# Performance work log

Measured on AMD Instinct MI355X. Metric: run time of the kernel, lower is better.

## Reference

```python
import jax, jax.numpy as jnp
import numpy as np

N_NODES = 50000
N_EDGES = 800000
OUT_DIM = 394
BN_EPS = 1e-5


def setup_inputs() -> dict:
    key = jax.random.key(0)
    ks = jax.random.split(key, 10)
    x = jax.random.normal(ks[0], (N_NODES, 2), dtype=jnp.float32)
    edge_index = jax.random.randint(ks[1], (2, N_EDGES), 0, N_NODES, dtype=jnp.int64)
    W_gcn = jax.random.normal(ks[2], (OUT_DIM, 2), dtype=jnp.float32) * 0.5
    b_gcn = jax.random.normal(ks[3], (OUT_DIM,), dtype=jnp.float32) * 0.1
    bn_gamma = jax.random.normal(ks[4], (OUT_DIM,), dtype=jnp.float32) * 0.1 + 1.0
    bn_beta = jax.random.normal(ks[5], (OUT_DIM,), dtype=jnp.float32) * 0.1
    bn_mean = jax.random.normal(ks[6], (OUT_DIM,), dtype=jnp.float32) * 0.1
    bn_var = jax.random.uniform(ks[7], (OUT_DIM,), dtype=jnp.float32, minval=0.5, maxval=1.5)
    fc_w = jax.random.normal(ks[8], (OUT_DIM, OUT_DIM), dtype=jnp.float32) * (1.0 / np.sqrt(OUT_DIM))
    fc_b = jax.random.normal(ks[9], (OUT_DIM,), dtype=jnp.float32) * 0.1
    return {"x": x, "edge_index": edge_index, "W_gcn": W_gcn, "b_gcn": b_gcn,
            "bn_gamma": bn_gamma, "bn_beta": bn_beta, "bn_mean": bn_mean,
            "bn_var": bn_var, "fc_w": fc_w, "fc_b": fc_b}


def reference(x, edge_index, W_gcn, b_gcn, bn_gamma, bn_beta, bn_mean, bn_var, fc_w, fc_b):
    n = x.shape[0]
    loop = jnp.arange(n, dtype=edge_index.dtype)
    # PyG GCNConv: add self-loops, symmetric deg^{-1/2} normalization
    src = jnp.concatenate([edge_index[0], loop])  # [E+N] message sources
    dst = jnp.concatenate([edge_index[1], loop])  # [E+N] message targets
    deg = jax.ops.segment_sum(jnp.ones_like(dst, dtype=x.dtype), dst, num_segments=n)
    dinv = jnp.where(deg > 0, jax.lax.rsqrt(deg), 0.0)
    norm = dinv[src] * dinv[dst]  # [E+N]
    xl = x @ W_gcn.T  # [N, 394] linear transform before aggregation
    msgs = xl[src] * norm[:, None]  # [E+N, 394] gathered + normalized messages
    agg = jax.ops.segment_sum(msgs, dst, num_segments=n) + b_gcn  # scatter-add
    h = jax.nn.relu(agg)
    # BatchNorm1d in eval mode (running stats)
    h = (h - bn_mean) * jax.lax.rsqrt(bn_var + BN_EPS) * bn_gamma + bn_beta
    # dropout is a no-op in eval mode
    z = h @ fc_w.T + fc_b
    return (jax.nn.log_softmax(z, axis=1), z)
```

## Files before the change

kernel.cpp:

```cpp
#include <hip/hip_runtime.h>
#include <math.h>

#define DIM 394
#define KP  416
#define NT  13
#define NP  448
#define BN_EPS 1e-5f
#define MAXD 32

typedef __bf16 bf16x8 __attribute__((ext_vector_type(8)));
typedef float  f32x4  __attribute__((ext_vector_type(4)));

__device__ inline bool edges_are_int32(const int* ei) {
    int l = threadIdx.x & 63;
    unsigned long long b = __ballot(ei[2 * l + 1] != 0);
    return b != 0ULL;
}


__global__ void place_pack_kernel(const int* __restrict__ ei,
                                  unsigned* __restrict__ degc,
                                  unsigned* __restrict__ payload,
                                  unsigned* __restrict__ ocnt,
                                  uint2* __restrict__ olist, int e, int eb4,
                                  const float* __restrict__ Wg,
                                  const float* __restrict__ bg,
                                  const float* __restrict__ gamma,
                                  const float* __restrict__ beta,
                                  const float* __restrict__ mean,
                                  const float* __restrict__ var,
                                  const float* __restrict__ fcw,
                                  float4* __restrict__ Pk, float* __restrict__ Ok,
                                  bf16x8* __restrict__ Bp) {
    int b = blockIdx.x, t = threadIdx.x;
    if (b < eb4) {
        bool is32 = edges_are_int32(ei);
        int i0 = (b * 256 + t) * 4;
        if (i0 >= e) return;
        int s[4], d[4];
        int cnt = 4;
        if (i0 + 4 <= e) {
            if (is32) {
                int4 sv = *reinterpret_cast<const int4*>(&ei[i0]);
                int4 dv = *reinterpret_cast<const int4*>(&ei[e + i0]);
                s[0] = sv.x; s[1] = sv.y; s[2] = sv.z; s[3] = sv.w;
                d[0] = dv.x; d[1] = dv.y; d[2] = dv.z; d[3] = dv.w;
            } else {
                int4 a = *reinterpret_cast<const int4*>(&ei[2 * i0]);
                int4 bb = *reinterpret_cast<const int4*>(&ei[2 * i0 + 4]);
                int4 c = *reinterpret_cast<const int4*>(&ei[2 * (e + i0)]);
                int4 dd = *reinterpret_cast<const int4*>(&ei[2 * (e + i0) + 4]);
                s[0] = a.x; s[1] = a.z; s[2] = bb.x; s[3] = bb.z;
                d[0] = c.x; d[1] = c.z; d[2] = dd.x; d[3] = dd.z;
            }
        } else {
            cnt = e - i0;
            for (int j = 0; j < cnt; ++j) {
                s[j] = is32 ? ei[i0 + j]     : ei[2 * (i0 + j)];
                d[j] = is32 ? ei[e + i0 + j] : ei[2 * (e + i0 + j)];
            }
        }
        #pragma unroll
        for (int j = 0; j < 4; ++j) {
            if (j >= cnt) break;
            unsigned tk = atomicAdd(&degc[d[j]], 1u);
            if (tk < MAXD) {
                payload[(size_t)d[j] * MAXD + tk] = (unsigned)s[j];
            } else {
                unsigned o = atomicAdd(ocnt, 1u);
                olist[o] = make_uint2((unsigned)s[j], (unsigned)d[j]);
            }
        }
    } else if (b < eb4 + 2) {
        int k = (b - eb4) * 256 + t;
        if (k < KP) {
            float4 p = make_float4(0.f, 0.f, 0.f, 0.f);
            float o = 0.f;
            if (k < DIM) {
                p.x = Wg[2 * k];
                p.y = Wg[2 * k + 1];
                p.z = bg[k];
                float sc = gamma[k] * rsqrtf(var[k] + BN_EPS);
                p.w = sc;
                o = beta[k] - sc * mean[k];
            }
            Pk[k] = p;
            Ok[k] = o;
        }
    } else {
        int idx = (b - eb4 - 2) * 256 + t;
        if (idx < NT * 4 * NP) {
            int col = idx % NP;
            int r   = idx / NP;
            int k0  = r * 8;
            bf16x8 v;
            #pragma unroll
            for (int q = 0; q < 8; ++q) {
                int k = k0 + q;
                float f = (col < DIM && k < DIM) ? fcw[col * DIM + k] : 0.0f;
                v[q] = (__bf16)f;
            }
            Bp[idx] = v;
        }
    }
}

__global__ __launch_bounds__(256, 2)
void gemm_fused(const float2* __restrict__ x2, const unsigned* __restrict__ degc,
                const unsigned* __restrict__ payload,
                const unsigned* __restrict__ ocnt, const uint2* __restrict__ olist,
                const float4* __restrict__ Pk, const float* __restrict__ Ok,
                const bf16x8* __restrict__ Bp, const float* __restrict__ fcb,
                float* __restrict__ outp, float* __restrict__ z, int n) {
    __shared__ bf16x8 As[2][256];
    __shared__ float2 red[64][4];

    int tid = threadIdx.x;
    int wv  = tid >> 6;
    int l   = tid & 63;
    int cg_ = tid & 15;
    int kg  = l >> 4;
    int row0 = blockIdx.x * 64;
    int gi = row0 + l;

    float y0 = 0.f, y1 = 0.f;
    {
        float2 psum = make_float2(0.f, 0.f);
        float dinv_i = 0.f;
        float2 xi = make_float2(0.f, 0.f);
        if (gi < n) {
            unsigned dg = degc[gi];
            dinv_i = rsqrtf(1.0f + (float)dg);
            xi = x2[gi];
            unsigned m = dg < MAXD ? dg : MAXD;
            const unsigned* pl = payload + (size_t)gi * MAXD;
            for (unsigned t = wv; t < m; t += 4) {
                unsigned s = pl[t];
                float2 xv = x2[s];
                float ds = rsqrtf(1.0f + (float)degc[s]);
                psum.x = fmaf(ds, xv.x, psum.x);
                psum.y = fmaf(ds, xv.y, psum.y);
            }
            if (wv == 0) {
                unsigned cnt = *ocnt;
                for (unsigned j = 0; j < cnt; ++j) {
                    uint2 sd = olist[j];
                    if ((int)sd.y == gi) {
                        float2 xv = x2[sd.x];
                        float ds = rsqrtf(1.0f + (float)degc[sd.x]);
                        psum.x = fmaf(ds, xv.x, psum.x);
                        psum.y = fmaf(ds, xv.y, psum.y);
                    }
                }
            }
        }
        red[l][wv] = psum;
        __syncthreads();
        if (gi < n) {
            float sx = red[l][0].x + red[l][1].x + red[l][2].x + red[l][3].x;
            float sy = red[l][0].y + red[l][1].y + red[l][2].y + red[l][3].y;
            y0 = dinv_i * (sx + dinv_i * xi.x);
            y1 = dinv_i * (sy + dinv_i * xi.y);
        }
    }

    f32x4 acc[4][7];
    #pragma unroll
    for (int a = 0; a < 4; ++a)
        #pragma unroll
        for (int b = 0; b < 7; ++b)
            acc[a][b] = (f32x4){0.f, 0.f, 0.f, 0.f};

    auto stageA = [&](int ks, int buf) {
        int kb = ks * 32 + wv * 8;
        bf16x8 hv;
        #pragma unroll
        for (int q = 0; q < 8; ++q) {
            float4 p = Pk[kb + q];
            float t = fmaf(y0, p.x, fmaf(y1, p.y, p.z));
            t = fmaxf(t, 0.f);
            hv[q] = (__bf16)fmaf(p.w, t, Ok[kb + q]);
        }
        As[buf][wv * 64 + l] = hv;
    };

    const bf16x8* bptr = Bp + (kg * 448 + wv * 112 + cg_);

    bf16x8 Bcur[7], Bnxt[7];
    #pragma unroll
    for (int c = 0; c < 7; ++c) Bcur[c] = bptr[c * 16];
    stageA(0, 0);
    __syncthreads();

    int buf = 0;
    for (int ks = 0; ks < NT; ++ks) {
        if (ks < NT - 1) {
            const bf16x8* bn = bptr + (size_t)(ks + 1) * (4 * 448);
            #pragma unroll
            for (int c = 0; c < 7; ++c) Bnxt[c] = bn[c * 16];
            stageA(ks + 1, buf ^ 1);
        }
        bf16x8 af[4];
        #pragma unroll
        for (int rt = 0; rt < 4; ++rt)
            af[rt] = As[buf][kg * 64 + rt * 16 + cg_];
        #pragma unroll
        for (int ct = 0; ct < 7; ++ct)
            #pragma unroll
            for (int rt = 0; rt < 4; ++rt)
                acc[rt][ct] = __builtin_amdgcn_mfma_f32_16x16x32_bf16(
                                  af[rt], Bcur[ct], acc[rt][ct], 0, 0, 0);
        __syncthreads();
        #pragma unroll
        for (int c = 0; c < 7; ++c) Bcur[c] = Bnxt[c];
        buf ^= 1;
    }

    float* redm = (float*)&As[0][0];
    float* reds = redm + 256;

    int colb = wv * 112;
    float bias[7];
    bool  cv[7];
    #pragma unroll
    for (int ct = 0; ct < 7; ++ct) {
        int c = colb + ct * 16 + cg_;
        cv[ct] = (c < DIM);
        bias[ct] = cv[ct] ? fcb[c] : 0.f;
    }
    #pragma unroll
    for (int rt = 0; rt < 4; ++rt)
        #pragma unroll
        for (int ct = 0; ct < 7; ++ct)
            acc[rt][ct] = acc[rt][ct] + bias[ct];

    f32x4 mx[4];
    #pragma unroll
    for (int rt = 0; rt < 4; ++rt) {
        f32x4 m = (f32x4){-1e30f, -1e30f, -1e30f, -1e30f};
        #pragma unroll
        for (int ct = 0; ct < 7; ++ct) {
            if (!cv[ct]) continue;
            #pragma unroll
            for (int j = 0; j < 4; ++j) m[j] = fmaxf(m[j], acc[rt][ct][j]);
        }
        #pragma unroll
        for (int msk = 1; msk < 16; msk <<= 1)
            #pragma unroll
            for (int j = 0; j < 4; ++j)
                m[j] = fmaxf(m[j], __shfl_xor(m[j], msk));
        mx[rt] = m;
    }
    if (cg_ == 0) {
        #pragma unroll
        for (int rt = 0; rt < 4; ++rt)
            #pragma unroll
            for (int j = 0; j < 4; ++j)
                redm[(rt * 16 + kg * 4 + j) * 4 + wv] = mx[rt][j];
    }
    __syncthreads();
    f32x4 gm[4];
    #pragma unroll
    for (int rt = 0; rt < 4; ++rt)
        #pragma unroll
        for (int j = 0; j < 4; ++j) {
            int r = (rt * 16 + kg * 4 + j) * 4;
            gm[rt][j] = fmaxf(fmaxf(redm[r], redm[r + 1]),
                              fmaxf(redm[r + 2], redm[r + 3]));
        }

    f32x4 sm[4];
    #pragma unroll
    for (int rt = 0; rt < 4; ++rt) {
        f32x4 s = (f32x4){0.f, 0.f, 0.f, 0.f};
        #pragma unroll
        for (int ct = 0; ct < 7; ++ct) {
            if (!cv[ct]) continue;
            #pragma unroll
            for (int j = 0; j < 4; ++j)
                s[j] += __expf(acc[rt][ct][j] - gm[rt][j]);
        }
        #pragma unroll
        for (int msk = 1; msk < 16; msk <<= 1)
            #pragma unroll
            for (int j = 0; j < 4; ++j)
                s[j] += __shfl_xor(s[j], msk);
        sm[rt] = s;
    }
    if (cg_ == 0) {
        #pragma unroll
        for (int rt = 0; rt < 4; ++rt)
            #pragma unroll
            for (int j = 0; j < 4; ++j)
                reds[(rt * 16 + kg * 4 + j) * 4 + wv] = sm[rt][j];
    }
    __syncthreads();
    f32x4 lse[4];
    #pragma unroll
    for (int rt = 0; rt < 4; ++rt)
        #pragma unroll
        for (int j = 0; j < 4; ++j) {
            int r = (rt * 16 + kg * 4 + j) * 4;
            float t = reds[r] + reds[r + 1] + reds[r + 2] + reds[r + 3];
            lse[rt][j] = gm[rt][j] + __logf(t);
        }

    #pragma unroll
    for (int rt = 0; rt < 4; ++rt)
        #pragma unroll
        for (int j = 0; j < 4; ++j) {
            int grow = row0 + rt * 16 + kg * 4 + j;
            if (grow >= n) continue;
            size_t base = (size_t)grow * DIM;
            float L = lse[rt][j];
            #pragma unroll
            for (int ct = 0; ct < 7; ++ct) {
                if (!cv[ct]) continue;
                int c = colb + ct * 16 + cg_;
                float zv = acc[rt][ct][j];
                z[base + c]    = zv;
                outp[base + c] = zv - L;
            }
        }
}

extern "C" void kernel_launch(void* const* d_in, const int* in_sizes, int n_in,
                              void* d_out, int out_size, void* d_ws, size_t ws_size,
                              hipStream_t stream) {
    int n = in_sizes[0] / 2;
    int e = in_sizes[1] / 2;

    const float2* x2   = (const float2*)d_in[0];
    const int*   ei    = (const int*)d_in[1];
    const float* Wg    = (const float*)d_in[2];
    const float* bg    = (const float*)d_in[3];
    const float* gamma = (const float*)d_in[4];
    const float* beta  = (const float*)d_in[5];
    const float* mean  = (const float*)d_in[6];
    const float* var   = (const float*)d_in[7];
    const float* fcw   = (const float*)d_in[8];
    const float* fcb   = (const float*)d_in[9];

    float* out = (float*)d_out;
    float* z   = out + (size_t)n * DIM;

    char* wsb = (char*)d_ws;
    unsigned* degc  = (unsigned*)wsb;
    unsigned* ocnt  = (unsigned*)(degc + n);
    uint2*    olist = (uint2*)(ocnt + 4);
    size_t off = (size_t)(n + 4) * 4 + (size_t)e * 8;
    off = (off + 255) & ~(size_t)255;
    unsigned* payload = (unsigned*)(wsb + off);
    off += (size_t)n * MAXD * 4;
    off = (off + 255) & ~(size_t)255;
    bf16x8* Bp = (bf16x8*)(wsb + off);
    off += (size_t)NT * 4 * NP * 16;
    float4* Pk = (float4*)(wsb + off);
    off += (size_t)KP * 16;
    float* Ok  = (float*)(wsb + off);

    hipMemsetAsync(degc, 0, (size_t)(n + 4) * 4, stream);

    int eb4 = (e / 4 + 255) / 256 + 1;
    int pack_blocks = 2 + (NT * 4 * NP + 255) / 256;
    place_pack_kernel<<<eb4 + pack_blocks, 256, 0, stream>>>(
        ei, degc, payload, ocnt, olist, e, eb4,
        Wg, bg, gamma, beta, mean, var, fcw, Pk, Ok, Bp);

    int gm = (n + 63) / 64;
    gemm_fused<<<gm, 256, 0, stream>>>(x2, degc, payload, ocnt, olist,
                                       Pk, Ok, Bp, fcb, out, z, n);
}
```

Before: 139.9 us.

## Scatter overflow edges in separate kernel and stage output through LDS for coalesced stores

Overflow edges (degree beyond MAXD) are no longer scanned linearly by every row in the GEMM kernel. A new cleanup kernel atomically adds their contributions into a per-node yover buffer, which the GEMM reads directly. The epilogue also transposes each 16-row tile through shared memory so z and log-softmax outputs are written as contiguous float2 row segments instead of strided scalar stores. This adds a kernel launch, a larger memset and extra barriers, and the larger shared footprint may reduce occupancy.

```diff
diff --git a/kernel.cpp b/kernel.cpp
--- a/kernel.cpp
+++ b/kernel.cpp
@@ -7,6 +7,7 @@
 #define NP  448
 #define BN_EPS 1e-5f
 #define MAXD 32
+#define TST 452
 
 typedef __bf16 bf16x8 __attribute__((ext_vector_type(8)));
 typedef float  f32x4  __attribute__((ext_vector_type(4)));
@@ -105,15 +106,33 @@
     }
 }
 
+__global__ void cleanup_kernel(const uint2* __restrict__ olist,
+                               const unsigned* __restrict__ ocnt,
+                               const unsigned* __restrict__ degc,
+                               const float2* __restrict__ x2,
+                               float* __restrict__ yover) {
+    unsigned cnt = *ocnt;
+    int gstride = gridDim.x * blockDim.x;
+    for (unsigned i = blockIdx.x * blockDim.x + threadIdx.x; i < cnt; i += gstride) {
+        uint2 sd = olist[i];
+        float ds = rsqrtf(1.0f + (float)degc[sd.x]);
+        float2 xv = x2[sd.x];
+        atomicAdd(&yover[2 * sd.y],     ds * xv.x);
+        atomicAdd(&yover[2 * sd.y + 1], ds * xv.y);
+    }
+}
+
 __global__ __launch_bounds__(256, 2)
 void gemm_fused(const float2* __restrict__ x2, const unsigned* __restrict__ degc,
-                const unsigned* __restrict__ payload,
-                const unsigned* __restrict__ ocnt, const uint2* __restrict__ olist,
+                const unsigned* __restrict__ payload, const float* __restrict__ yover,
                 const float4* __restrict__ Pk, const float* __restrict__ Ok,
                 const bf16x8* __restrict__ Bp, const float* __restrict__ fcb,
                 float* __restrict__ outp, float* __restrict__ z, int n) {
-    __shared__ bf16x8 As[2][256];
-    __shared__ float2 red[64][4];
+    __shared__ alignas(16) char smem[16 * TST * 4 + 64];
+    bf16x8* As   = (bf16x8*)smem;
+    float2* red  = (float2*)(smem + 8192);
+    float*  T    = (float*)smem;
+    float*  lsebuf = (float*)(smem + 16 * TST * 4);
 
     int tid = threadIdx.x;
     int wv  = tid >> 6;
@@ -142,26 +161,19 @@
                 psum.y = fmaf(ds, xv.y, psum.y);
             }
             if (wv == 0) {
-                unsigned cnt = *ocnt;
-                for (unsigned j = 0; j < cnt; ++j) {
-                    uint2 sd = olist[j];
-                    if ((int)sd.y == gi) {
-                        float2 xv = x2[sd.x];
-                        float ds = rsqrtf(1.0f + (float)degc[sd.x]);
-                        psum.x = fmaf(ds, xv.x, psum.x);
-                        psum.y = fmaf(ds, xv.y, psum.y);
-                    }
-                }
-            }
-        }
-        red[l][wv] = psum;
+                psum.x += yover[2 * gi];
+                psum.y += yover[2 * gi + 1];
+            }
+        }
+        red[l * 4 + wv] = psum;
         __syncthreads();
         if (gi < n) {
-            float sx = red[l][0].x + red[l][1].x + red[l][2].x + red[l][3].x;
-            float sy = red[l][0].y + red[l][1].y + red[l][2].y + red[l][3].y;
+            float sx = red[l * 4 + 0].x + red[l * 4 + 1].x + red[l * 4 + 2].x + red[l * 4 + 3].x;
+            float sy = red[l * 4 + 0].y + red[l * 4 + 1].y + red[l * 4 + 2].y + red[l * 4 + 3].y;
             y0 = dinv_i * (sx + dinv_i * xi.x);
             y1 = dinv_i * (sy + dinv_i * xi.y);
         }
+        __syncthreads();
     }
 
     f32x4 acc[4][7];
@@ -181,7 +193,7 @@
             t = fmaxf(t, 0.f);
             hv[q] = (__bf16)fmaf(p.w, t, Ok[kb + q]);
         }
-        As[buf][wv * 64 + l] = hv;
+        As[buf * 256 + wv * 64 + l] = hv;
     };
 
     const bf16x8* bptr = Bp + (kg * 448 + wv * 112 + cg_);
@@ -203,7 +215,7 @@
         bf16x8 af[4];
         #pragma unroll
         for (int rt = 0; rt < 4; ++rt)
-            af[rt] = As[buf][kg * 64 + rt * 16 + cg_];
+            af[rt] = As[buf * 256 + kg * 64 + rt * 16 + cg_];
         #pragma unroll
         for (int ct = 0; ct < 7; ++ct)
             #pragma unroll
@@ -216,7 +228,7 @@
         buf ^= 1;
     }
 
-    float* redm = (float*)&As[0][0];
+    float* redm = (float*)smem;
     float* reds = redm + 256;
 
     int colb = wv * 112;
@@ -304,24 +316,46 @@
             float t = reds[r] + reds[r + 1] + reds[r + 2] + reds[r + 3];
             lse[rt][j] = gm[rt][j] + __logf(t);
         }
-
-    #pragma unroll
-    for (int rt = 0; rt < 4; ++rt)
-        #pragma unroll
-        for (int j = 0; j < 4; ++j) {
-            int grow = row0 + rt * 16 + kg * 4 + j;
-            if (grow >= n) continue;
-            size_t base = (size_t)grow * DIM;
-            float L = lse[rt][j];
-            #pragma unroll
-            for (int ct = 0; ct < 7; ++ct) {
-                if (!cv[ct]) continue;
-                int c = colb + ct * 16 + cg_;
-                float zv = acc[rt][ct][j];
-                z[base + c]    = zv;
-                outp[base + c] = zv - L;
-            }
-        }
+    __syncthreads();
+
+    #pragma unroll
+    for (int rt = 0; rt < 4; ++rt) {
+        #pragma unroll
+        for (int ct = 0; ct < 7; ++ct) {
+            int c = colb + ct * 16 + cg_;
+            #pragma unroll
+            for (int j = 0; j < 4; ++j)
+                T[(kg * 4 + j) * TST + c] = acc[rt][ct][j];
+        }
+        if (wv == 0 && cg_ == 0) {
+            #pragma unroll
+            for (int j = 0; j < 4; ++j)
+                lsebuf[kg * 4 + j] = lse[rt][j];
+        }
+        __syncthreads();
+        #pragma unroll
+        for (int q = 0; q < 7; ++q) {
+            int idx = tid + q * 256;
+            int row = idx / 112;
+            int c4  = idx - row * 112;
+            int grow2 = row0 + rt * 16 + row;
+            if (grow2 < n && c4 <= 98) {
+                float4 v = *reinterpret_cast<const float4*>(&T[row * TST + c4 * 4]);
+                float L = lsebuf[row];
+                size_t base = (size_t)grow2 * DIM + c4 * 4;
+                if (c4 <= 97) {
+                    *reinterpret_cast<float2*>(&z[base])        = make_float2(v.x, v.y);
+                    *reinterpret_cast<float2*>(&z[base + 2])    = make_float2(v.z, v.w);
+                    *reinterpret_cast<float2*>(&outp[base])     = make_float2(v.x - L, v.y - L);
+                    *reinterpret_cast<float2*>(&outp[base + 2]) = make_float2(v.z - L, v.w - L);
+                } else {
+                    *reinterpret_cast<float2*>(&z[base])    = make_float2(v.x, v.y);
+                    *reinterpret_cast<float2*>(&outp[base]) = make_float2(v.x - L, v.y - L);
+                }
+            }
+        }
+        __syncthreads();
+    }
 }
 
 extern "C" void kernel_launch(void* const* d_in, const int* in_sizes, int n_in,
@@ -346,9 +380,10 @@
 
     char* wsb = (char*)d_ws;
     unsigned* degc  = (unsigned*)wsb;
-    unsigned* ocnt  = (unsigned*)(degc + n);
+    float*    yover = (float*)(degc + n);
+    unsigned* ocnt  = (unsigned*)(yover + 2 * (size_t)n);
     uint2*    olist = (uint2*)(ocnt + 4);
-    size_t off = (size_t)(n + 4) * 4 + (size_t)e * 8;
+    size_t off = (size_t)(3 * n + 4) * 4 + (size_t)e * 8;
     off = (off + 255) & ~(size_t)255;
     unsigned* payload = (unsigned*)(wsb + off);
     off += (size_t)n * MAXD * 4;
@@ -359,15 +394,16 @@
     off += (size_t)KP * 16;
     float* Ok  = (float*)(wsb + off);
 
-    hipMemsetAsync(degc, 0, (size_t)(n + 4) * 4, stream);
+    hipMemsetAsync(degc, 0, (size_t)(3 * n + 4) * 4, stream);
 
     int eb4 = (e / 4 + 255) / 256 + 1;
     int pack_blocks = 2 + (NT * 4 * NP + 255) / 256;
     place_pack_kernel<<<eb4 + pack_blocks, 256, 0, stream>>>(
         ei, degc, payload, ocnt, olist, e, eb4,
         Wg, bg, gamma, beta, mean, var, fcw, Pk, Ok, Bp);
+    cleanup_kernel<<<64, 256, 0, stream>>>(olist, ocnt, degc, x2, yover);
 
     int gm = (n + 63) / 64;
-    gemm_fused<<<gm, 256, 0, stream>>>(x2, degc, payload, ocnt, olist,
+    gemm_fused<<<gm, 256, 0, stream>>>(x2, degc, payload, yover,
                                        Pk, Ok, Bp, fcb, out, z, n);
 }
```

New measurement: 139.3 us. About the same (-0.4%).
